# Kernel optimization log

Measured on AMD Instinct MI355X. Metric: run time of the kernel, lower is better.

The kernel has to match this reference:

```python
import jax, jax.numpy as jnp
import numpy as np

ATT = 256
NUM_GENES = 2128
HIDDEN = 512
B, T = 128, 1024


def setup_inputs() -> dict:
    key = jax.random.key(0)
    ks = jax.random.split(key, 8)
    return {
        "genes": jax.random.normal(ks[0], (B, NUM_GENES), dtype=jnp.float32),
        "smiles": jax.random.normal(ks[1], (B, T, HIDDEN), dtype=jnp.float32),
        "w_num_gene_features": jax.random.normal(ks[2], (1,), dtype=jnp.float32) * 0.1,
        "w_genes": jax.random.normal(ks[3], (NUM_GENES, ATT), dtype=jnp.float32) * 0.1,
        "b_genes": jax.random.normal(ks[4], (ATT,), dtype=jnp.float32) * 0.1,
        "dense_kernel": jax.random.normal(ks[5], (HIDDEN, ATT), dtype=jnp.float32) * 0.05,
        "dense_bias": jnp.zeros((ATT,), dtype=jnp.float32),
        "v": jax.random.normal(ks[6], (ATT,), dtype=jnp.float32) * 0.1,
    }


def reference(genes, smiles, w_num_gene_features, w_genes, b_genes,
              dense_kernel, dense_bias, v):
    # genes: [B, G]; collapse trivial feature axis via scalar weight -> [B, G]
    genes_collapsed = genes * w_num_gene_features[0]
    # gene context: [B, A]
    gene_proj = genes_collapsed @ w_genes + b_genes
    # smiles projection: [B, T, A]
    smiles_proj = jnp.einsum('bth,ha->bta', smiles, dense_kernel) + dense_bias
    # additive attention energies
    x = jnp.tanh(gene_proj[:, None, :] + smiles_proj)          # [B, T, A]
    xv = jnp.einsum('bta,a->bt', x, v)                          # [B, T]
    alphas = jax.nn.softmax(xv, axis=-1)                        # [B, T]
    output = jnp.einsum('bth,bt->bh', smiles, alphas)           # [B, H]
    return output, alphas
```

## Files before the change

kernel.cpp:

```cpp
#include <hip/hip_runtime.h>
#include <stdint.h>

#define B_ 128
#define T_ 1024
#define H_ 512
#define A_ 256
#define G_ 2128

typedef short s16x8 __attribute__((ext_vector_type(8)));
typedef float f32x4 __attribute__((ext_vector_type(4)));

__device__ inline unsigned short f2bf(float f) {
  unsigned u = __float_as_uint(f);
  u += 0x7fff + ((u >> 16) & 1);
  return (unsigned short)(u >> 16);
}
__device__ inline unsigned pack2bf(float a, float b) {
  return ((unsigned)f2bf(b) << 16) | f2bf(a);
}
__device__ inline float fast_tanh(float x) {
  x = fminf(15.f, fmaxf(-15.f, x));
  float e = __expf(2.f * x);
  return (e - 1.f) * __builtin_amdgcn_rcpf(e + 1.f);
}

__global__ void prep_kt(const float* __restrict__ K,
                        unsigned short* __restrict__ khi) {
  int idx = blockIdx.x * 256 + threadIdx.x;
  int h = idx >> 8;
  int a = idx & 255;
  khi[(h >> 5) * 8192 + a * 32 + (h & 31)] = f2bf(K[idx]);
}

__global__ __launch_bounds__(256) void gene_proj_k(
    const float* __restrict__ genes, const float* __restrict__ w0p,
    const float* __restrict__ Wg, const float* __restrict__ bg,
    const float* __restrict__ db, float* __restrict__ gp) {
  int b = blockIdx.x;
  int a = threadIdx.x;
  const float* gb = genes + (size_t)b * G_;
  float s = 0.f;
  #pragma unroll 4
  for (int g4 = 0; g4 < G_ / 4; ++g4) {
    float4 gv = *reinterpret_cast<const float4*>(gb + g4 * 4);
    s = fmaf(gv.x, Wg[(g4 * 4 + 0) * A_ + a], s);
    s = fmaf(gv.y, Wg[(g4 * 4 + 1) * A_ + a], s);
    s = fmaf(gv.z, Wg[(g4 * 4 + 2) * A_ + a], s);
    s = fmaf(gv.w, Wg[(g4 * 4 + 3) * A_ + a], s);
  }
  gp[b * A_ + a] = w0p[0] * s + bg[a] + db[a];
}

__global__ __launch_bounds__(256, 4) void pass1(
    const float* __restrict__ smiles, const unsigned short* __restrict__ khi,
    const float* __restrict__ gp, const float* __restrict__ v,
    float* __restrict__ xv) {
  __shared__ unsigned short sA[64 * 32];
  __shared__ unsigned short sB[256 * 32];
  __shared__ float sXV[64 * 4];

  const int tid = threadIdx.x;
  const int b = blockIdx.y;
  const int t0 = blockIdx.x * 64;
  const int lane = tid & 63;
  const int w = tid >> 6;
  const int n = lane & 15;
  const int q = lane >> 4;

  const float* sb = smiles + ((size_t)b * T_ + t0) * H_;

  f32x4 acc[4][4];
  #pragma unroll
  for (int i = 0; i < 4; ++i)
    #pragma unroll
    for (int j = 0; j < 4; ++j)
      acc[i][j] = (f32x4){0.f, 0.f, 0.f, 0.f};

  const int ar = tid >> 2;
  const int ac = tid & 3;
  const int swA = (ac ^ (ar & 3)) * 8;
  const int swB0 = (0 ^ (tid & 3)) * 8;
  const int swB1 = (1 ^ (tid & 3)) * 8;
  const int swB2 = (2 ^ (tid & 3)) * 8;
  const int swB3 = (3 ^ (tid & 3)) * 8;

  for (int kb = 0; kb < 16; ++kb) {
    const int k0 = kb * 32;
    __syncthreads();
    {
      const float* src = sb + ar * H_ + k0 + ac * 8;
      float4 f0 = *reinterpret_cast<const float4*>(src);
      float4 f1 = *reinterpret_cast<const float4*>(src + 4);
      uint4 p;
      p.x = pack2bf(f0.x, f0.y); p.y = pack2bf(f0.z, f0.w);
      p.z = pack2bf(f1.x, f1.y); p.w = pack2bf(f1.z, f1.w);
      *reinterpret_cast<uint4*>(&sA[ar * 32 + swA]) = p;
    }
    {
      const uint4* src = reinterpret_cast<const uint4*>(khi + kb * 8192 + tid * 32);
      uint4 q0 = src[0], q1 = src[1], q2 = src[2], q3 = src[3];
      unsigned short* row = &sB[tid * 32];
      *reinterpret_cast<uint4*>(row + swB0) = q0;
      *reinterpret_cast<uint4*>(row + swB1) = q1;
      *reinterpret_cast<uint4*>(row + swB2) = q2;
      *reinterpret_cast<uint4*>(row + swB3) = q3;
    }
    __syncthreads();

    s16x8 af[4], bh[4];
    const int sw = (q ^ (n & 3)) * 8;
    #pragma unroll
    for (int i = 0; i < 4; ++i)
      af[i] = *reinterpret_cast<const s16x8*>(&sA[(i * 16 + n) * 32 + sw]);
    #pragma unroll
    for (int j = 0; j < 4; ++j)
      bh[j] = *reinterpret_cast<const s16x8*>(&sB[(w * 64 + j * 16 + n) * 32 + sw]);
    #pragma unroll
    for (int i = 0; i < 4; ++i)
      #pragma unroll
      for (int j = 0; j < 4; ++j)
        acc[i][j] = __builtin_amdgcn_mfma_f32_16x16x32_bf16(af[i], bh[j], acc[i][j], 0, 0, 0);
  }

  float vv[4], gg[4];
  #pragma unroll
  for (int j = 0; j < 4; ++j) {
    int a = w * 64 + j * 16 + n;
    vv[j] = v[a];
    gg[j] = gp[b * A_ + a];
  }
  #pragma unroll
  for (int i = 0; i < 4; ++i) {
    #pragma unroll
    for (int r = 0; r < 4; ++r) {
      float s = 0.f;
      #pragma unroll
      for (int j = 0; j < 4; ++j)
        s += vv[j] * fast_tanh(acc[i][j][r] + gg[j]);
      s += __shfl_xor(s, 1); s += __shfl_xor(s, 2);
      s += __shfl_xor(s, 4); s += __shfl_xor(s, 8);
      if (n == 0) sXV[(i * 16 + q * 4 + r) * 4 + w] = s;
    }
  }
  __syncthreads();
  if (tid < 64) {
    float* p = &sXV[tid * 4];
    xv[(size_t)b * T_ + t0 + tid] = p[0] + p[1] + p[2] + p[3];
  }
}

__global__ __launch_bounds__(256) void softmax_k(const float* __restrict__ xv,
                                                 float* __restrict__ alphas) {
  __shared__ float red[8];
  int b = blockIdx.x, tid = threadIdx.x;
  float4 x = *reinterpret_cast<const float4*>(xv + b * T_ + tid * 4);
  float m = fmaxf(fmaxf(x.x, x.y), fmaxf(x.z, x.w));
  #pragma unroll
  for (int o = 1; o < 64; o <<= 1) m = fmaxf(m, __shfl_xor(m, o));
  if ((tid & 63) == 0) red[tid >> 6] = m;
  __syncthreads();
  m = fmaxf(fmaxf(red[0], red[1]), fmaxf(red[2], red[3]));
  float e0 = __expf(x.x - m), e1 = __expf(x.y - m);
  float e2 = __expf(x.z - m), e3 = __expf(x.w - m);
  float s = e0 + e1 + e2 + e3;
  #pragma unroll
  for (int o = 1; o < 64; o <<= 1) s += __shfl_xor(s, o);
  if ((tid & 63) == 0) red[4 + (tid >> 6)] = s;
  __syncthreads();
  s = red[4] + red[5] + red[6] + red[7];
  float inv = 1.f / s;
  float4 o4;
  o4.x = e0 * inv; o4.y = e1 * inv; o4.z = e2 * inv; o4.w = e3 * inv;
  *reinterpret_cast<float4*>(alphas + b * T_ + tid * 4) = o4;
}

__global__ __launch_bounds__(256) void pass3(const float* __restrict__ smiles,
                                             const float* __restrict__ alphas,
                                             float* __restrict__ out) {
  int b = blockIdx.y;
  int t0 = blockIdx.x * 64;
  int tid = threadIdx.x;
  int tg = tid >> 7;
  int h4 = (tid & 127) * 4;
  const float* sb = smiles + (size_t)b * T_ * H_;
  f32x4 acc = (f32x4){0.f, 0.f, 0.f, 0.f};
  #pragma unroll 8
  for (int i = 0; i < 32; ++i) {
    int t = t0 + 2 * i + tg;
    float al = alphas[b * T_ + t];
    float4 sv = *reinterpret_cast<const float4*>(sb + (size_t)t * H_ + h4);
    acc.x = fmaf(al, sv.x, acc.x); acc.y = fmaf(al, sv.y, acc.y);
    acc.z = fmaf(al, sv.z, acc.z); acc.w = fmaf(al, sv.w, acc.w);
  }
  float* op = out + b * H_ + h4;
  atomicAdd(op + 0, acc.x); atomicAdd(op + 1, acc.y);
  atomicAdd(op + 2, acc.z); atomicAdd(op + 3, acc.w);
}

extern "C" void kernel_launch(void* const* d_in, const int* in_sizes, int n_in,
                              void* d_out, int out_size, void* d_ws, size_t ws_size,
                              hipStream_t stream) {
  const float* genes  = (const float*)d_in[0];
  const float* smiles = (const float*)d_in[1];
  const float* w0     = (const float*)d_in[2];
  const float* wg     = (const float*)d_in[3];
  const float* bg     = (const float*)d_in[4];
  const float* dk     = (const float*)d_in[5];
  const float* db     = (const float*)d_in[6];
  const float* v      = (const float*)d_in[7];
  float* out = (float*)d_out;
  char* ws = (char*)d_ws;
  float* gp = (float*)ws;
  unsigned short* khi = (unsigned short*)(ws + 131072);
  float* xv = (float*)(ws + 131072 + 262144);
  float* alphas = out + B_ * H_;

  hipMemsetAsync(out, 0, B_ * H_ * sizeof(float), stream);
  prep_kt<<<512, 256, 0, stream>>>(dk, khi);
  gene_proj_k<<<B_, 256, 0, stream>>>(genes, w0, wg, bg, db, gp);
  pass1<<<dim3(T_ / 64, B_), 256, 0, stream>>>(smiles, khi, gp, v, xv);
  softmax_k<<<B_, 256, 0, stream>>>(xv, alphas);
  pass3<<<dim3(16, B_), 256, 0, stream>>>(smiles, alphas, out);
}
```

Before: 526.6 us.

## Pre-convert smiles to swizzled bf16 tiles and load via global_load_lds

Adds a conversion pass that writes smiles once as bf16 in a tiled, pre-swizzled layout. pass1 then streams A and B tiles directly into LDS with global_load_lds, and pass3 reads the half-size bf16 copy with an in-block reduction before the atomics. The weight prep now applies the same swizzle, and gene_proj is split across four blocks per batch that combine with atomics. The extra conversion pass adds a full read and write of smiles, and the weighted sum now uses bf16 inputs, which costs accuracy.

New measurement: 527.2 us. About the same (+0.1%).

```diff
diff --git a/kernel.cpp b/kernel.cpp
--- a/kernel.cpp
+++ b/kernel.cpp
@@ -9,6 +9,7 @@
 
 typedef short s16x8 __attribute__((ext_vector_type(8)));
 typedef float f32x4 __attribute__((ext_vector_type(4)));
+typedef unsigned int u32;
 
 __device__ inline unsigned short f2bf(float f) {
   unsigned u = __float_as_uint(f);
@@ -18,10 +19,17 @@
 __device__ inline unsigned pack2bf(float a, float b) {
   return ((unsigned)f2bf(b) << 16) | f2bf(a);
 }
+__device__ inline float bf_lo(unsigned u) { return __uint_as_float(u << 16); }
+__device__ inline float bf_hi(unsigned u) { return __uint_as_float(u & 0xffff0000u); }
 __device__ inline float fast_tanh(float x) {
   x = fminf(15.f, fmaxf(-15.f, x));
   float e = __expf(2.f * x);
   return (e - 1.f) * __builtin_amdgcn_rcpf(e + 1.f);
+}
+__device__ inline void gl_lds16(const void* g, void* l) {
+  __builtin_amdgcn_global_load_lds(
+      (const __attribute__((address_space(1))) u32*)g,
+      (__attribute__((address_space(3))) u32*)l, 16, 0, 0);
 }
 
 __global__ void prep_kt(const float* __restrict__ K,
@@ -29,30 +37,51 @@
   int idx = blockIdx.x * 256 + threadIdx.x;
   int h = idx >> 8;
   int a = idx & 255;
-  khi[(h >> 5) * 8192 + a * 32 + (h & 31)] = f2bf(K[idx]);
+  int kb = h >> 5, k = h & 31;
+  int grp = k >> 3, sub = k & 7;
+  khi[kb * 8192 + a * 32 + ((grp ^ (a & 3)) * 8) + sub] = f2bf(K[idx]);
+}
+
+__global__ __launch_bounds__(256) void convert_k(const float* __restrict__ smiles,
+                                                 unsigned short* __restrict__ smb) {
+  int f = blockIdx.x * 256 + threadIdx.x;
+  int h8 = f & 63;
+  int t = (f >> 6) & 1023;
+  int b = f >> 16;
+  const float* src = smiles + ((size_t)(b * 1024 + t)) * 512 + h8 * 8;
+  float4 a0 = *reinterpret_cast<const float4*>(src);
+  float4 a1 = *reinterpret_cast<const float4*>(src + 4);
+  uint4 p;
+  p.x = pack2bf(a0.x, a0.y); p.y = pack2bf(a0.z, a0.w);
+  p.z = pack2bf(a1.x, a1.y); p.w = pack2bf(a1.z, a1.w);
+  int tb = t >> 6, tp = t & 63, kb = h8 >> 2, g = h8 & 3;
+  size_t dst = ((((size_t)b * 16 + tb) * 16 + kb) * 64 + tp) * 32
+             + ((g ^ (tp & 3)) * 8);
+  *reinterpret_cast<uint4*>(smb + dst) = p;
 }
 
 __global__ __launch_bounds__(256) void gene_proj_k(
     const float* __restrict__ genes, const float* __restrict__ w0p,
     const float* __restrict__ Wg, const float* __restrict__ bg,
     const float* __restrict__ db, float* __restrict__ gp) {
+  __shared__ float sg[532];
   int b = blockIdx.x;
+  int gc = blockIdx.y;
   int a = threadIdx.x;
-  const float* gb = genes + (size_t)b * G_;
+  int g0 = gc * 532;
+  for (int i = threadIdx.x; i < 532; i += 256) sg[i] = genes[(size_t)b * G_ + g0 + i];
+  __syncthreads();
   float s = 0.f;
-  #pragma unroll 4
-  for (int g4 = 0; g4 < G_ / 4; ++g4) {
-    float4 gv = *reinterpret_cast<const float4*>(gb + g4 * 4);
-    s = fmaf(gv.x, Wg[(g4 * 4 + 0) * A_ + a], s);
-    s = fmaf(gv.y, Wg[(g4 * 4 + 1) * A_ + a], s);
-    s = fmaf(gv.z, Wg[(g4 * 4 + 2) * A_ + a], s);
-    s = fmaf(gv.w, Wg[(g4 * 4 + 3) * A_ + a], s);
-  }
-  gp[b * A_ + a] = w0p[0] * s + bg[a] + db[a];
+  #pragma unroll 8
+  for (int g = 0; g < 532; ++g)
+    s = fmaf(sg[g], Wg[(size_t)(g0 + g) * A_ + a], s);
+  float val = w0p[0] * s;
+  if (gc == 0) val += bg[a] + db[a];
+  atomicAdd(&gp[b * A_ + a], val);
 }
 
 __global__ __launch_bounds__(256, 4) void pass1(
-    const float* __restrict__ smiles, const unsigned short* __restrict__ khi,
+    const unsigned short* __restrict__ smb, const unsigned short* __restrict__ khi,
     const float* __restrict__ gp, const float* __restrict__ v,
     float* __restrict__ xv) {
   __shared__ unsigned short sA[64 * 32];
@@ -61,13 +90,13 @@
 
   const int tid = threadIdx.x;
   const int b = blockIdx.y;
-  const int t0 = blockIdx.x * 64;
+  const int tb = blockIdx.x;
   const int lane = tid & 63;
   const int w = tid >> 6;
   const int n = lane & 15;
   const int q = lane >> 4;
 
-  const float* sb = smiles + ((size_t)b * T_ + t0) * H_;
+  const unsigned short* Ab = smb + (((size_t)b * 16 + tb) * 16) * 2048;
 
   f32x4 acc[4][4];
   #pragma unroll
@@ -76,35 +105,13 @@
     for (int j = 0; j < 4; ++j)
       acc[i][j] = (f32x4){0.f, 0.f, 0.f, 0.f};
 
-  const int ar = tid >> 2;
-  const int ac = tid & 3;
-  const int swA = (ac ^ (ar & 3)) * 8;
-  const int swB0 = (0 ^ (tid & 3)) * 8;
-  const int swB1 = (1 ^ (tid & 3)) * 8;
-  const int swB2 = (2 ^ (tid & 3)) * 8;
-  const int swB3 = (3 ^ (tid & 3)) * 8;
-
   for (int kb = 0; kb < 16; ++kb) {
-    const int k0 = kb * 32;
     __syncthreads();
-    {
-      const float* src = sb + ar * H_ + k0 + ac * 8;
-      float4 f0 = *reinterpret_cast<const float4*>(src);
-      float4 f1 = *reinterpret_cast<const float4*>(src + 4);
-      uint4 p;
-      p.x = pack2bf(f0.x, f0.y); p.y = pack2bf(f0.z, f0.w);
-      p.z = pack2bf(f1.x, f1.y); p.w = pack2bf(f1.z, f1.w);
-      *reinterpret_cast<uint4*>(&sA[ar * 32 + swA]) = p;
-    }
-    {
-      const uint4* src = reinterpret_cast<const uint4*>(khi + kb * 8192 + tid * 32);
-      uint4 q0 = src[0], q1 = src[1], q2 = src[2], q3 = src[3];
-      unsigned short* row = &sB[tid * 32];
-      *reinterpret_cast<uint4*>(row + swB0) = q0;
-      *reinterpret_cast<uint4*>(row + swB1) = q1;
-      *reinterpret_cast<uint4*>(row + swB2) = q2;
-      *reinterpret_cast<uint4*>(row + swB3) = q3;
-    }
+    gl_lds16(Ab + kb * 2048 + w * 512 + lane * 8, &sA[w * 512]);
+    #pragma unroll
+    for (int r = 0; r < 4; ++r)
+      gl_lds16(khi + kb * 8192 + w * 2048 + r * 512 + lane * 8,
+               &sB[w * 2048 + r * 512]);
     __syncthreads();
 
     s16x8 af[4], bh[4];
@@ -145,7 +152,7 @@
   __syncthreads();
   if (tid < 64) {
     float* p = &sXV[tid * 4];
-    xv[(size_t)b * T_ + t0 + tid] = p[0] + p[1] + p[2] + p[3];
+    xv[(size_t)b * T_ + tb * 64 + tid] = p[0] + p[1] + p[2] + p[3];
   }
 }
 
@@ -174,27 +181,40 @@
   *reinterpret_cast<float4*>(alphas + b * T_ + tid * 4) = o4;
 }
 
-__global__ __launch_bounds__(256) void pass3(const float* __restrict__ smiles,
+__global__ __launch_bounds__(256) void pass3(const unsigned short* __restrict__ smb,
                                              const float* __restrict__ alphas,
                                              float* __restrict__ out) {
-  int b = blockIdx.y;
-  int t0 = blockIdx.x * 64;
+  __shared__ float red[3][64][8];
+  int b = blockIdx.y, ts = blockIdx.x;
   int tid = threadIdx.x;
-  int tg = tid >> 7;
-  int h4 = (tid & 127) * 4;
-  const float* sb = smiles + (size_t)b * T_ * H_;
-  f32x4 acc = (f32x4){0.f, 0.f, 0.f, 0.f};
-  #pragma unroll 8
-  for (int i = 0; i < 32; ++i) {
-    int t = t0 + 2 * i + tg;
-    float al = alphas[b * T_ + t];
-    float4 sv = *reinterpret_cast<const float4*>(sb + (size_t)t * H_ + h4);
-    acc.x = fmaf(al, sv.x, acc.x); acc.y = fmaf(al, sv.y, acc.y);
-    acc.z = fmaf(al, sv.z, acc.z); acc.w = fmaf(al, sv.w, acc.w);
-  }
-  float* op = out + b * H_ + h4;
-  atomicAdd(op + 0, acc.x); atomicAdd(op + 1, acc.y);
-  atomicAdd(op + 2, acc.z); atomicAdd(op + 3, acc.w);
+  int hg = tid & 63, tq = tid >> 6;
+  int kb = hg >> 2, g = hg & 3;
+  float acc[8] = {0.f, 0.f, 0.f, 0.f, 0.f, 0.f, 0.f, 0.f};
+  for (int tb = ts * 4; tb < ts * 4 + 4; ++tb) {
+    const unsigned short* tile = smb + (((size_t)b * 16 + tb) * 16 + kb) * 2048;
+    const float* al = alphas + b * T_ + tb * 64;
+    #pragma unroll 4
+    for (int tt = 0; tt < 16; ++tt) {
+      int tp = tq * 16 + tt;
+      float a = al[tp];
+      uint4 d = *reinterpret_cast<const uint4*>(tile + tp * 32 + ((g ^ (tp & 3)) * 8));
+      acc[0] = fmaf(a, bf_lo(d.x), acc[0]); acc[1] = fmaf(a, bf_hi(d.x), acc[1]);
+      acc[2] = fmaf(a, bf_lo(d.y), acc[2]); acc[3] = fmaf(a, bf_hi(d.y), acc[3]);
+      acc[4] = fmaf(a, bf_lo(d.z), acc[4]); acc[5] = fmaf(a, bf_hi(d.z), acc[5]);
+      acc[6] = fmaf(a, bf_lo(d.w), acc[6]); acc[7] = fmaf(a, bf_hi(d.w), acc[7]);
+    }
+  }
+  if (tq) {
+    #pragma unroll
+    for (int e = 0; e < 8; ++e) red[tq - 1][hg][e] = acc[e];
+  }
+  __syncthreads();
+  if (tq == 0) {
+    float* op = out + (size_t)b * H_ + kb * 32 + g * 8;
+    #pragma unroll
+    for (int e = 0; e < 8; ++e)
+      atomicAdd(op + e, acc[e] + red[0][hg][e] + red[1][hg][e] + red[2][hg][e]);
+  }
 }
 
 extern "C" void kernel_launch(void* const* d_in, const int* in_sizes, int n_in,
@@ -213,12 +233,15 @@
   float* gp = (float*)ws;
   unsigned short* khi = (unsigned short*)(ws + 131072);
   float* xv = (float*)(ws + 131072 + 262144);
+  unsigned short* smb = (unsigned short*)(ws + (1 << 20));
   float* alphas = out + B_ * H_;
 
+  hipMemsetAsync(gp, 0, B_ * A_ * sizeof(float), stream);
   hipMemsetAsync(out, 0, B_ * H_ * sizeof(float), stream);
   prep_kt<<<512, 256, 0, stream>>>(dk, khi);
-  gene_proj_k<<<B_, 256, 0, stream>>>(genes, w0, wg, bg, db, gp);
-  pass1<<<dim3(T_ / 64, B_), 256, 0, stream>>>(smiles, khi, gp, v, xv);
+  convert_k<<<32768, 256, 0, stream>>>(smiles, smb);
+  gene_proj_k<<<dim3(B_, 4), 256, 0, stream>>>(genes, w0, wg, bg, db, gp);
+  pass1<<<dim3(16, B_), 256, 0, stream>>>(smb, khi, gp, v, xv);
   softmax_k<<<B_, 256, 0, stream>>>(xv, alphas);
-  pass3<<<dim3(16, B_), 256, 0, stream>>>(smiles, alphas, out);
-}
+  pass3<<<dim3(4, B_), 256, 0, stream>>>(smb, alphas, out);
+}
```
